# Kernel optimization log

Hardware: AMD Instinct MI355X
Metric: run time of the kernel (lower is better)

Reference implementation:

```python
import jax, jax.numpy as jnp
import numpy as np

D_LOGIC = 256
D_MEMORY = 256
NHEAD = 4
B, S = 2, 4096


def setup_inputs() -> dict:
    key = jax.random.key(0)
    ks = jax.random.split(key, 12)
    scale = 0.02
    x_logic = jax.random.normal(ks[0], (B, S, D_LOGIC), dtype=jnp.float32)
    x_memory = jax.random.normal(ks[1], (B, S, D_MEMORY), dtype=jnp.float32)
    mask = jax.random.randint(ks[2], (1, 1, S, S), 0, 2, dtype=jnp.int32)
    # torch nn.Linear weights are [out_features, in_features]
    Wq = jax.random.normal(ks[3], (D_LOGIC, D_LOGIC), dtype=jnp.float32) * scale
    bq = jnp.zeros((D_LOGIC,), dtype=jnp.float32)
    Wk = jax.random.normal(ks[4], (D_LOGIC, D_LOGIC), dtype=jnp.float32) * scale
    bk = jnp.zeros((D_LOGIC,), dtype=jnp.float32)
    Wv = jax.random.normal(ks[5], (D_MEMORY, D_MEMORY), dtype=jnp.float32) * scale
    bv = jnp.zeros((D_MEMORY,), dtype=jnp.float32)
    Wo = jax.random.normal(ks[6], (D_MEMORY, D_MEMORY), dtype=jnp.float32) * scale
    bo = jnp.zeros((D_MEMORY,), dtype=jnp.float32)
    return {"x_logic": x_logic, "x_memory": x_memory, "mask": mask,
            "Wq": Wq, "bq": bq, "Wk": Wk, "bk": bk,
            "Wv": Wv, "bv": bv, "Wo": Wo, "bo": bo}


def reference(x_logic, x_memory, mask, Wq, bq, Wk, bk, Wv, bv, Wo, bo):
    batch, seq, _ = x_logic.shape
    hd_l = D_LOGIC // NHEAD   # head_dim_logic
    hd_m = D_MEMORY // NHEAD  # head_dim_memory
    # Q, K from logic stream
    Q = (x_logic @ Wq.T + bq).reshape(batch, seq, NHEAD, hd_l)
    K = (x_logic @ Wk.T + bk).reshape(batch, seq, NHEAD, hd_l)
    # scores: [B, H, S, S]
    scores = jnp.einsum('bqhd,bkhd->bhqk', Q, K) / jnp.sqrt(jnp.float32(hd_l))
    scores = jnp.where(mask == 0, jnp.float32(-1e9), scores)
    attn = jax.nn.softmax(scores, axis=-1)
    # V from memory stream
    V = (x_memory @ Wv.T + bv).reshape(batch, seq, NHEAD, hd_m)
    out = jnp.einsum('bhqk,bkhd->bqhd', attn, V).reshape(batch, seq, D_MEMORY)
    return out @ Wo.T + bo
```

## Files before the change

kernel.cpp:

```cpp
#include <hip/hip_runtime.h>

#define S_  4096
#define HD_ 64
#define H_  4
#define B_  2
#define DM  256
#define NS  4
#define KSPAN (S_ / NS)
#define NITER (KSPAN / 64)

typedef __bf16 bf16x8 __attribute__((ext_vector_type(8)));
typedef __bf16 bf16x4 __attribute__((ext_vector_type(4)));
typedef float  f32x4  __attribute__((ext_vector_type(4)));
typedef unsigned long long u64;

__device__ __forceinline__ bf16x8 cvt8(const float* p) {
    float4 u0 = *reinterpret_cast<const float4*>(p);
    float4 u1 = *reinterpret_cast<const float4*>(p + 4);
    bf16x8 r = { (__bf16)u0.x, (__bf16)u0.y, (__bf16)u0.z, (__bf16)u0.w,
                 (__bf16)u1.x, (__bf16)u1.y, (__bf16)u1.z, (__bf16)u1.w };
    return r;
}

__global__ __launch_bounds__(256) void pack_kernel(const int* __restrict__ mask,
                                                   u64* __restrict__ packed,
                                                   const float* __restrict__ Wq,
                                                   const float* __restrict__ Wk,
                                                   const float* __restrict__ Wv,
                                                   const float* __restrict__ Wo,
                                                   __bf16* __restrict__ wqb,
                                                   __bf16* __restrict__ wkb,
                                                   __bf16* __restrict__ wvb,
                                                   __bf16* __restrict__ wob) {
    const int bid = blockIdx.x;
    if (bid < 1024) {
        const int gw   = bid * 4 + (threadIdx.x >> 6);
        const int lane = threadIdx.x & 63;
        const int r  = lane >> 4;
        const int ll = lane & 15;
#pragma unroll
        for (int s = 0; s < 16; ++s) {
            const int u   = gw + s * 4096;
            const int kbb = u & 63;
            const int q0  = (u >> 6) * 4;
            const int4 v = *reinterpret_cast<const int4*>(
                mask + (size_t)(q0 + r) * S_ + kbb * 64 + ll * 4);
            const u64 b0 = __ballot(v.x != 0);
            const u64 b1 = __ballot(v.y != 0);
            const u64 b2 = __ballot(v.z != 0);
            const u64 b3 = __ballot(v.w != 0);
            if (ll == 0) {
                const u64 word = ((b0 >> (16 * r)) & 0xFFFFull)
                               | (((b1 >> (16 * r)) & 0xFFFFull) << 16)
                               | (((b2 >> (16 * r)) & 0xFFFFull) << 32)
                               | (((b3 >> (16 * r)) & 0xFFFFull) << 48);
                packed[(size_t)kbb * S_ + q0 + r] = word;
            }
        }
        return;
    }
    const int t = (bid - 1024) * 256 + threadIdx.x;
#pragma unroll
    for (int j = 0; j < 4; ++j) {
        const int idx = t + j * 16384;
        const int arr = idx >> 14, k = idx & 16383;
        const float* src = arr == 0 ? Wq : arr == 1 ? Wk : arr == 2 ? Wv : Wo;
        __bf16* dst      = arr == 0 ? wqb : arr == 1 ? wkb : arr == 2 ? wvb : wob;
        float4 v = reinterpret_cast<const float4*>(src)[k];
        bf16x4 o = { (__bf16)v.x, (__bf16)v.y, (__bf16)v.z, (__bf16)v.w };
        reinterpret_cast<bf16x4*>(dst)[k] = o;
    }
}

__global__ __launch_bounds__(256) void proj_qkv_kernel(const float* __restrict__ xl,
                                                       const float* __restrict__ xm,
                                                       const __bf16* __restrict__ wqb,
                                                       const __bf16* __restrict__ wkb,
                                                       const __bf16* __restrict__ wvb,
                                                       const float* __restrict__ bq,
                                                       const float* __restrict__ bk,
                                                       const float* __restrict__ bv,
                                                       __bf16* __restrict__ Qb,
                                                       __bf16* __restrict__ Kb,
                                                       __bf16* __restrict__ Vtb) {
    const int mode = blockIdx.z;
    const int ny   = blockIdx.y;
    const float*  X    = (mode == 2) ? xm : xl;
    const __bf16* W    = (mode == 0) ? wqb : (mode == 1) ? wkb : wvb;
    const float*  bias = (mode == 0) ? bq : (mode == 1) ? bk : bv;
    const float scale  = (mode == 0) ? 0.18033688011112042f : 1.0f;

    const int wid  = threadIdx.x >> 6;
    const int lane = threadIdx.x & 63;
    const int g = lane >> 4, c = lane & 15;
    const int m0 = blockIdx.x * 64 + wid * 16;
    const float* Xp = X + (size_t)m0 * DM;

    f32x4 acc[8];
#pragma unroll
    for (int i = 0; i < 8; ++i) acc[i] = (f32x4){0.f, 0.f, 0.f, 0.f};

#pragma unroll
    for (int kf = 0; kf < 8; ++kf) {
        bf16x8 a = cvt8(Xp + c * DM + kf * 32 + g * 8);
#pragma unroll
        for (int nt = 0; nt < 8; ++nt) {
            bf16x8 b = *reinterpret_cast<const bf16x8*>(
                W + (size_t)(ny * 128 + nt * 16 + c) * DM + kf * 32 + g * 8);
            acc[nt] = __builtin_amdgcn_mfma_f32_16x16x32_bf16(a, b, acc[nt], 0, 0, 0);
        }
    }

#pragma unroll
    for (int nt = 0; nt < 8; ++nt) {
        const int n = ny * 128 + nt * 16 + c;
        const float bs = bias[n];
        const int h = n >> 6, d = n & 63;
#pragma unroll
        for (int r = 0; r < 4; ++r) {
            const int m = m0 + g * 4 + r;
            const float v = (acc[nt][r] + bs) * scale;
            const int b_ = m >> 12, s = m & (S_ - 1);
            if (mode == 0)
                Qb[((size_t)(b_ * H_ + h) * S_ + s) * HD_ + d] = (__bf16)v;
            else if (mode == 1)
                Kb[((size_t)(b_ * H_ + h) * S_ + s) * HD_ + d] = (__bf16)v;
            else
                Vtb[((size_t)(b_ * H_ + h) * HD_ + d) * S_ + s] = (__bf16)v;
        }
    }
}

__global__ __launch_bounds__(256, 4) void attn_kernel(const __bf16* __restrict__ Q,
                                                      const __bf16* __restrict__ K,
                                                      const __bf16* __restrict__ Vt,
                                                      const u64* __restrict__ packed,
                                                      __bf16* __restrict__ Opart,
                                                      float* __restrict__ Lpart) {
    __shared__ __bf16 Kt[64][72];
    __shared__ __bf16 Vl[64][72];
    __shared__ __bf16 Pl[4][16][72];

    const int bh = blockIdx.x;
    const int sp = blockIdx.y;
    const int qt = blockIdx.z;
    const int tid  = threadIdx.x;
    const int wid  = tid >> 6;
    const int lane = tid & 63;
    const int g = lane >> 4, c = lane & 15;
    const int q0w = qt * 64 + wid * 16;

    const __bf16* Qp = Q + ((size_t)bh * S_ + q0w) * HD_;
    bf16x8 qb0 = *reinterpret_cast<const bf16x8*>(Qp + c * HD_ + g * 8);
    bf16x8 qb1 = *reinterpret_cast<const bf16x8*>(Qp + c * HD_ + 32 + g * 8);

    const __bf16* Kp = K  + (size_t)bh * S_ * HD_;
    const __bf16* Vp = Vt + (size_t)bh * HD_ * S_;

    const int srow = tid >> 2;
    const int sseg = (tid & 3) * 16;

    f32x4 o[4];
#pragma unroll
    for (int i = 0; i < 4; ++i) o[i] = (f32x4){0.f, 0.f, 0.f, 0.f};
    float rs = 0.f;

    const int k0 = sp * KSPAN;

    bf16x8 kr0, kr1, vr0, vr1;
    {
        const __bf16* krow = Kp + (size_t)(k0 + srow) * HD_ + sseg;
        const __bf16* vrow = Vp + (size_t)srow * S_ + k0 + sseg;
        kr0 = *reinterpret_cast<const bf16x8*>(krow);
        kr1 = *reinterpret_cast<const bf16x8*>(krow + 8);
        vr0 = *reinterpret_cast<const bf16x8*>(vrow);
        vr1 = *reinterpret_cast<const bf16x8*>(vrow + 8);
        *reinterpret_cast<bf16x8*>(&Kt[srow][sseg])     = kr0;
        *reinterpret_cast<bf16x8*>(&Kt[srow][sseg + 8]) = kr1;
        *reinterpret_cast<bf16x8*>(&Vl[srow][sseg])     = vr0;
        *reinterpret_cast<bf16x8*>(&Vl[srow][sseg + 8]) = vr1;
    }
    __syncthreads();

    for (int it = 0; it < NITER; ++it) {
        const int kb = k0 + it * 64;
        const bool more = (it + 1 < NITER);
        if (more) {
            const __bf16* krow = Kp + (size_t)(kb + 64 + srow) * HD_ + sseg;
            const __bf16* vrow = Vp + (size_t)srow * S_ + kb + 64 + sseg;
            kr0 = *reinterpret_cast<const bf16x8*>(krow);
            kr1 = *reinterpret_cast<const bf16x8*>(krow + 8);
            vr0 = *reinterpret_cast<const bf16x8*>(vrow);
            vr1 = *reinterpret_cast<const bf16x8*>(vrow + 8);
        }

        const u64 mw = packed[(size_t)(kb >> 6) * S_ + q0w + c];
        const unsigned wlo = (unsigned)mw, whi = (unsigned)(mw >> 32);

        f32x4 st[4];
#pragma unroll
        for (int nt = 0; nt < 4; ++nt) {
            bf16x8 ka0 = *reinterpret_cast<const bf16x8*>(&Kt[nt * 16 + c][g * 8]);
            bf16x8 ka1 = *reinterpret_cast<const bf16x8*>(&Kt[nt * 16 + c][32 + g * 8]);
            f32x4 z = (f32x4){0.f, 0.f, 0.f, 0.f};
            st[nt] = __builtin_amdgcn_mfma_f32_16x16x32_bf16(ka0, qb0, z, 0, 0, 0);
            st[nt] = __builtin_amdgcn_mfma_f32_16x16x32_bf16(ka1, qb1, st[nt], 0, 0, 0);
        }

#pragma unroll
        for (int nt = 0; nt < 4; ++nt) {
            const unsigned sh = nt * 4 + g;
            float p0 = ((wlo >> sh) & 1u)        ? exp2f(st[nt][0]) : 0.f;
            float p1 = ((wlo >> (sh + 16)) & 1u) ? exp2f(st[nt][1]) : 0.f;
            float p2 = ((whi >> sh) & 1u)        ? exp2f(st[nt][2]) : 0.f;
            float p3 = ((whi >> (sh + 16)) & 1u) ? exp2f(st[nt][3]) : 0.f;
            rs += (p0 + p1) + (p2 + p3);
            bf16x4 pw = { (__bf16)p0, (__bf16)p1, (__bf16)p2, (__bf16)p3 };
            *reinterpret_cast<bf16x4*>(&Pl[wid][c][nt * 16 + g * 4]) = pw;
        }

        bf16x8 pa0 = *reinterpret_cast<const bf16x8*>(&Pl[wid][c][g * 8]);
        bf16x8 pa1 = *reinterpret_cast<const bf16x8*>(&Pl[wid][c][32 + g * 8]);

#pragma unroll
        for (int nt = 0; nt < 4; ++nt) {
            bf16x8 vb0 = *reinterpret_cast<const bf16x8*>(&Vl[nt * 16 + c][g * 8]);
            bf16x8 vb1 = *reinterpret_cast<const bf16x8*>(&Vl[nt * 16 + c][32 + g * 8]);
            o[nt] = __builtin_amdgcn_mfma_f32_16x16x32_bf16(pa0, vb0, o[nt], 0, 0, 0);
            o[nt] = __builtin_amdgcn_mfma_f32_16x16x32_bf16(pa1, vb1, o[nt], 0, 0, 0);
        }

        __syncthreads();
        if (more) {
            *reinterpret_cast<bf16x8*>(&Kt[srow][sseg])     = kr0;
            *reinterpret_cast<bf16x8*>(&Kt[srow][sseg + 8]) = kr1;
            *reinterpret_cast<bf16x8*>(&Vl[srow][sseg])     = vr0;
            *reinterpret_cast<bf16x8*>(&Vl[srow][sseg + 8]) = vr1;
            __syncthreads();
        }
    }

    rs += __shfl_xor(rs, 16);
    rs += __shfl_xor(rs, 32);
    if (lane < 16)
        Lpart[(size_t)(bh * NS + sp) * S_ + q0w + c] = rs;

    const size_t obase = ((size_t)(bh * NS + sp) * S_ + q0w) * 64;
#pragma unroll
    for (int nt = 0; nt < 4; ++nt) {
#pragma unroll
        for (int r = 0; r < 4; ++r)
            Opart[obase + (size_t)(g * 4 + r) * 64 + nt * 16 + c] = (__bf16)o[nt][r];
    }
}

__global__ __launch_bounds__(256) void proj_o_kernel(const __bf16* __restrict__ Opart,
                                                     const float* __restrict__ Lpart,
                                                     const __bf16* __restrict__ wob,
                                                     const float* __restrict__ bo,
                                                     float* __restrict__ out) {
    const int ny   = blockIdx.y;
    const int wid  = threadIdx.x >> 6;
    const int lane = threadIdx.x & 63;
    const int g = lane >> 4, c = lane & 15;
    const int m0 = blockIdx.x * 64 + wid * 16;

    const int row = m0 + c;
    const int b_ = row >> 12, s = row & (S_ - 1);

    f32x4 acc[8];
#pragma unroll
    for (int i = 0; i < 8; ++i) acc[i] = (f32x4){0.f, 0.f, 0.f, 0.f};

#pragma unroll
    for (int kf = 0; kf < 8; ++kf) {
        const int dcol = kf * 32 + g * 8;
        const int h = dcol >> 6, dm = dcol & 63;
        const int bh = b_ * H_ + h;
        float l = 0.f;
        float sum[8] = {0.f, 0.f, 0.f, 0.f, 0.f, 0.f, 0.f, 0.f};
#pragma unroll
        for (int sp = 0; sp < NS; ++sp) {
            l += Lpart[(size_t)(bh * NS + sp) * S_ + s];
            const size_t base = ((size_t)(bh * NS + sp) * S_ + s) * 64 + dm;
            bf16x8 p = *reinterpret_cast<const bf16x8*>(Opart + base);
#pragma unroll
            for (int j = 0; j < 8; ++j) sum[j] += (float)p[j];
        }
        const float invl = 1.0f / l;
        bf16x8 a = { (__bf16)(sum[0] * invl), (__bf16)(sum[1] * invl),
                     (__bf16)(sum[2] * invl), (__bf16)(sum[3] * invl),
                     (__bf16)(sum[4] * invl), (__bf16)(sum[5] * invl),
                     (__bf16)(sum[6] * invl), (__bf16)(sum[7] * invl) };
#pragma unroll
        for (int nt = 0; nt < 8; ++nt) {
            bf16x8 b = *reinterpret_cast<const bf16x8*>(
                wob + (size_t)(ny * 128 + nt * 16 + c) * DM + kf * 32 + g * 8);
            acc[nt] = __builtin_amdgcn_mfma_f32_16x16x32_bf16(a, b, acc[nt], 0, 0, 0);
        }
    }

#pragma unroll
    for (int nt = 0; nt < 8; ++nt) {
        const int n = ny * 128 + nt * 16 + c;
        const float bs = bo[n];
#pragma unroll
        for (int r = 0; r < 4; ++r) {
            const int m = m0 + g * 4 + r;
            out[(size_t)m * DM + n] = acc[nt][r] + bs;
        }
    }
}

extern "C" void kernel_launch(void* const* d_in, const int* in_sizes, int n_in,
                              void* d_out, int out_size, void* d_ws, size_t ws_size,
                              hipStream_t stream) {
    const float* x_logic  = (const float*)d_in[0];
    const float* x_memory = (const float*)d_in[1];
    const int*   mask     = (const int*)d_in[2];
    const float* Wq = (const float*)d_in[3];
    const float* bq = (const float*)d_in[4];
    const float* Wk = (const float*)d_in[5];
    const float* bk = (const float*)d_in[6];
    const float* Wv = (const float*)d_in[7];
    const float* bv = (const float*)d_in[8];
    const float* Wo = (const float*)d_in[9];
    const float* bo = (const float*)d_in[10];
    float* out = (float*)d_out;

    char* ws = (char*)d_ws;
    size_t off = 0;
    auto alloc = [&](size_t bytes) { char* p = ws + off; off += (bytes + 255) & ~255ull; return p; };

    const size_t NX = (size_t)B_ * S_ * DM;
    u64*    packed = (u64*)alloc((size_t)S_ * (S_ / 64) * 8);
    __bf16* wqb = (__bf16*)alloc((size_t)DM * DM * 2);
    __bf16* wkb = (__bf16*)alloc((size_t)DM * DM * 2);
    __bf16* wvb = (__bf16*)alloc((size_t)DM * DM * 2);
    __bf16* wob = (__bf16*)alloc((size_t)DM * DM * 2);
    __bf16* Qb  = (__bf16*)alloc(NX * 2);
    __bf16* Kb  = (__bf16*)alloc(NX * 2);
    __bf16* Vtb = (__bf16*)alloc(NX * 2);
    __bf16* Opart = (__bf16*)alloc((size_t)B_ * H_ * NS * S_ * HD_ * 2);
    float*  Lpart = (float*)alloc((size_t)B_ * H_ * NS * S_ * 4);

    pack_kernel<<<1088, 256, 0, stream>>>(mask, packed, Wq, Wk, Wv, Wo, wqb, wkb, wvb, wob);
    proj_qkv_kernel<<<dim3(128, 2, 3), 256, 0, stream>>>(x_logic, x_memory, wqb, wkb, wvb,
                                                         bq, bk, bv, Qb, Kb, Vtb);
    attn_kernel<<<dim3(8, NS, 64), 256, 0, stream>>>(Qb, Kb, Vtb, packed, Opart, Lpart);
    proj_o_kernel<<<dim3(128, 2), 256, 0, stream>>>(Opart, Lpart, wob, bo, out);
}
```

Measured before the change: 138.7 us.

## Double-buffer K/V tiles in LDS with one barrier per iteration

The attention kernel now keeps two LDS buffers for the K and V tiles. While the current tile is being computed, the next tile's registers are stored into the other buffer and the tile after that is prefetched from global memory. This cuts the barriers per iteration from two to one and gives global loads a longer lead time. It also adds s_setprio around the MFMA sections, and the mask pack kernel now batches four loads before doing the ballots. In exchange, LDS use doubles, which may reduce occupancy, and register pressure goes up.

```diff
diff --git a/kernel.cpp b/kernel.cpp
--- a/kernel.cpp
+++ b/kernel.cpp
@@ -39,22 +39,32 @@
         const int r  = lane >> 4;
         const int ll = lane & 15;
 #pragma unroll
-        for (int s = 0; s < 16; ++s) {
-            const int u   = gw + s * 4096;
-            const int kbb = u & 63;
-            const int q0  = (u >> 6) * 4;
-            const int4 v = *reinterpret_cast<const int4*>(
-                mask + (size_t)(q0 + r) * S_ + kbb * 64 + ll * 4);
-            const u64 b0 = __ballot(v.x != 0);
-            const u64 b1 = __ballot(v.y != 0);
-            const u64 b2 = __ballot(v.z != 0);
-            const u64 b3 = __ballot(v.w != 0);
-            if (ll == 0) {
-                const u64 word = ((b0 >> (16 * r)) & 0xFFFFull)
-                               | (((b1 >> (16 * r)) & 0xFFFFull) << 16)
-                               | (((b2 >> (16 * r)) & 0xFFFFull) << 32)
-                               | (((b3 >> (16 * r)) & 0xFFFFull) << 48);
-                packed[(size_t)kbb * S_ + q0 + r] = word;
+        for (int sb = 0; sb < 4; ++sb) {
+            int4 v[4];
+#pragma unroll
+            for (int j = 0; j < 4; ++j) {
+                const int u   = gw + (sb * 4 + j) * 4096;
+                const int kbb = u & 63;
+                const int q0  = (u >> 6) * 4;
+                v[j] = *reinterpret_cast<const int4*>(
+                    mask + (size_t)(q0 + r) * S_ + kbb * 64 + ll * 4);
+            }
+#pragma unroll
+            for (int j = 0; j < 4; ++j) {
+                const int u   = gw + (sb * 4 + j) * 4096;
+                const int kbb = u & 63;
+                const int q0  = (u >> 6) * 4;
+                const u64 b0 = __ballot(v[j].x != 0);
+                const u64 b1 = __ballot(v[j].y != 0);
+                const u64 b2 = __ballot(v[j].z != 0);
+                const u64 b3 = __ballot(v[j].w != 0);
+                if (ll == 0) {
+                    const u64 word = ((b0 >> (16 * r)) & 0xFFFFull)
+                                   | (((b1 >> (16 * r)) & 0xFFFFull) << 16)
+                                   | (((b2 >> (16 * r)) & 0xFFFFull) << 32)
+                                   | (((b3 >> (16 * r)) & 0xFFFFull) << 48);
+                    packed[(size_t)kbb * S_ + q0 + r] = word;
+                }
             }
         }
         return;
@@ -137,8 +147,8 @@
                                                       const u64* __restrict__ packed,
                                                       __bf16* __restrict__ Opart,
                                                       float* __restrict__ Lpart) {
-    __shared__ __bf16 Kt[64][72];
-    __shared__ __bf16 Vl[64][72];
+    __shared__ __bf16 Kt[2][64][72];
+    __shared__ __bf16 Vl[2][64][72];
     __shared__ __bf16 Pl[4][16][72];
 
     const int bh = blockIdx.x;
@@ -166,46 +176,60 @@
     float rs = 0.f;
 
     const int k0 = sp * KSPAN;
-
-    bf16x8 kr0, kr1, vr0, vr1;
+    const __bf16* kptr = Kp + (size_t)(k0 + srow) * HD_ + sseg;
+    const __bf16* vptr = Vp + (size_t)srow * S_ + k0 + sseg;
+
     {
-        const __bf16* krow = Kp + (size_t)(k0 + srow) * HD_ + sseg;
-        const __bf16* vrow = Vp + (size_t)srow * S_ + k0 + sseg;
-        kr0 = *reinterpret_cast<const bf16x8*>(krow);
-        kr1 = *reinterpret_cast<const bf16x8*>(krow + 8);
-        vr0 = *reinterpret_cast<const bf16x8*>(vrow);
-        vr1 = *reinterpret_cast<const bf16x8*>(vrow + 8);
-        *reinterpret_cast<bf16x8*>(&Kt[srow][sseg])     = kr0;
-        *reinterpret_cast<bf16x8*>(&Kt[srow][sseg + 8]) = kr1;
-        *reinterpret_cast<bf16x8*>(&Vl[srow][sseg])     = vr0;
-        *reinterpret_cast<bf16x8*>(&Vl[srow][sseg + 8]) = vr1;
-    }
+        bf16x8 a0 = *reinterpret_cast<const bf16x8*>(kptr);
+        bf16x8 a1 = *reinterpret_cast<const bf16x8*>(kptr + 8);
+        bf16x8 b0 = *reinterpret_cast<const bf16x8*>(vptr);
+        bf16x8 b1 = *reinterpret_cast<const bf16x8*>(vptr + 8);
+        *reinterpret_cast<bf16x8*>(&Kt[0][srow][sseg])     = a0;
+        *reinterpret_cast<bf16x8*>(&Kt[0][srow][sseg + 8]) = a1;
+        *reinterpret_cast<bf16x8*>(&Vl[0][srow][sseg])     = b0;
+        *reinterpret_cast<bf16x8*>(&Vl[0][srow][sseg + 8]) = b1;
+    }
+    kptr += (size_t)64 * HD_;
+    vptr += 64;
+    bf16x8 kr0 = *reinterpret_cast<const bf16x8*>(kptr);
+    bf16x8 kr1 = *reinterpret_cast<const bf16x8*>(kptr + 8);
+    bf16x8 vr0 = *reinterpret_cast<const bf16x8*>(vptr);
+    bf16x8 vr1 = *reinterpret_cast<const bf16x8*>(vptr + 8);
     __syncthreads();
 
     for (int it = 0; it < NITER; ++it) {
+        const int cur = it & 1;
         const int kb = k0 + it * 64;
-        const bool more = (it + 1 < NITER);
-        if (more) {
-            const __bf16* krow = Kp + (size_t)(kb + 64 + srow) * HD_ + sseg;
-            const __bf16* vrow = Vp + (size_t)srow * S_ + kb + 64 + sseg;
-            kr0 = *reinterpret_cast<const bf16x8*>(krow);
-            kr1 = *reinterpret_cast<const bf16x8*>(krow + 8);
-            vr0 = *reinterpret_cast<const bf16x8*>(vrow);
-            vr1 = *reinterpret_cast<const bf16x8*>(vrow + 8);
+
+        if (it + 1 < NITER) {
+            *reinterpret_cast<bf16x8*>(&Kt[cur ^ 1][srow][sseg])     = kr0;
+            *reinterpret_cast<bf16x8*>(&Kt[cur ^ 1][srow][sseg + 8]) = kr1;
+            *reinterpret_cast<bf16x8*>(&Vl[cur ^ 1][srow][sseg])     = vr0;
+            *reinterpret_cast<bf16x8*>(&Vl[cur ^ 1][srow][sseg + 8]) = vr1;
+        }
+        if (it + 2 < NITER) {
+            kptr += (size_t)64 * HD_;
+            vptr += 64;
+            kr0 = *reinterpret_cast<const bf16x8*>(kptr);
+            kr1 = *reinterpret_cast<const bf16x8*>(kptr + 8);
+            vr0 = *reinterpret_cast<const bf16x8*>(vptr);
+            vr1 = *reinterpret_cast<const bf16x8*>(vptr + 8);
         }
 
         const u64 mw = packed[(size_t)(kb >> 6) * S_ + q0w + c];
         const unsigned wlo = (unsigned)mw, whi = (unsigned)(mw >> 32);
 
         f32x4 st[4];
+        __builtin_amdgcn_s_setprio(1);
 #pragma unroll
         for (int nt = 0; nt < 4; ++nt) {
-            bf16x8 ka0 = *reinterpret_cast<const bf16x8*>(&Kt[nt * 16 + c][g * 8]);
-            bf16x8 ka1 = *reinterpret_cast<const bf16x8*>(&Kt[nt * 16 + c][32 + g * 8]);
+            bf16x8 ka0 = *reinterpret_cast<const bf16x8*>(&Kt[cur][nt * 16 + c][g * 8]);
+            bf16x8 ka1 = *reinterpret_cast<const bf16x8*>(&Kt[cur][nt * 16 + c][32 + g * 8]);
             f32x4 z = (f32x4){0.f, 0.f, 0.f, 0.f};
             st[nt] = __builtin_amdgcn_mfma_f32_16x16x32_bf16(ka0, qb0, z, 0, 0, 0);
             st[nt] = __builtin_amdgcn_mfma_f32_16x16x32_bf16(ka1, qb1, st[nt], 0, 0, 0);
         }
+        __builtin_amdgcn_s_setprio(0);
 
 #pragma unroll
         for (int nt = 0; nt < 4; ++nt) {
@@ -222,22 +246,17 @@
         bf16x8 pa0 = *reinterpret_cast<const bf16x8*>(&Pl[wid][c][g * 8]);
         bf16x8 pa1 = *reinterpret_cast<const bf16x8*>(&Pl[wid][c][32 + g * 8]);
 
+        __builtin_amdgcn_s_setprio(1);
 #pragma unroll
         for (int nt = 0; nt < 4; ++nt) {
-            bf16x8 vb0 = *reinterpret_cast<const bf16x8*>(&Vl[nt * 16 + c][g * 8]);
-            bf16x8 vb1 = *reinterpret_cast<const bf16x8*>(&Vl[nt * 16 + c][32 + g * 8]);
+            bf16x8 vb0 = *reinterpret_cast<const bf16x8*>(&Vl[cur][nt * 16 + c][g * 8]);
+            bf16x8 vb1 = *reinterpret_cast<const bf16x8*>(&Vl[cur][nt * 16 + c][32 + g * 8]);
             o[nt] = __builtin_amdgcn_mfma_f32_16x16x32_bf16(pa0, vb0, o[nt], 0, 0, 0);
             o[nt] = __builtin_amdgcn_mfma_f32_16x16x32_bf16(pa1, vb1, o[nt], 0, 0, 0);
         }
-
-        __syncthreads();
-        if (more) {
-            *reinterpret_cast<bf16x8*>(&Kt[srow][sseg])     = kr0;
-            *reinterpret_cast<bf16x8*>(&Kt[srow][sseg + 8]) = kr1;
-            *reinterpret_cast<bf16x8*>(&Vl[srow][sseg])     = vr0;
-            *reinterpret_cast<bf16x8*>(&Vl[srow][sseg + 8]) = vr1;
-            __syncthreads();
-        }
+        __builtin_amdgcn_s_setprio(0);
+
+        if (it + 1 < NITER) __syncthreads();
     }
 
     rs += __shfl_xor(rs, 16);
```

Result: slower. 144.8 us (+4.3%).

## Process two query sub-tiles per wave in attention and batch mask loads

Applied to the files above, without the earlier changes.

Each attention wave now handles 32 query rows instead of 16, so every K/V tile staged in shared memory feeds twice as many MFMAs. The grid's query dimension is halved to match. This cuts global-to-LDS traffic and sync overhead per unit of work, at the cost of more registers per wave and fewer blocks to spread across CUs. Separately, the mask-packing loop now issues four int4 loads before doing the ballots, giving more memory-level parallelism.

```diff
diff --git a/kernel.cpp b/kernel.cpp
--- a/kernel.cpp
+++ b/kernel.cpp
@@ -39,22 +39,32 @@
         const int r  = lane >> 4;
         const int ll = lane & 15;
 #pragma unroll
-        for (int s = 0; s < 16; ++s) {
-            const int u   = gw + s * 4096;
-            const int kbb = u & 63;
-            const int q0  = (u >> 6) * 4;
-            const int4 v = *reinterpret_cast<const int4*>(
-                mask + (size_t)(q0 + r) * S_ + kbb * 64 + ll * 4);
-            const u64 b0 = __ballot(v.x != 0);
-            const u64 b1 = __ballot(v.y != 0);
-            const u64 b2 = __ballot(v.z != 0);
-            const u64 b3 = __ballot(v.w != 0);
-            if (ll == 0) {
-                const u64 word = ((b0 >> (16 * r)) & 0xFFFFull)
-                               | (((b1 >> (16 * r)) & 0xFFFFull) << 16)
-                               | (((b2 >> (16 * r)) & 0xFFFFull) << 32)
-                               | (((b3 >> (16 * r)) & 0xFFFFull) << 48);
-                packed[(size_t)kbb * S_ + q0 + r] = word;
+        for (int sb = 0; sb < 4; ++sb) {
+            int4 v[4];
+#pragma unroll
+            for (int j = 0; j < 4; ++j) {
+                const int u   = gw + (sb * 4 + j) * 4096;
+                const int kbb = u & 63;
+                const int q0  = (u >> 6) * 4;
+                v[j] = *reinterpret_cast<const int4*>(
+                    mask + (size_t)(q0 + r) * S_ + kbb * 64 + ll * 4);
+            }
+#pragma unroll
+            for (int j = 0; j < 4; ++j) {
+                const int u   = gw + (sb * 4 + j) * 4096;
+                const int kbb = u & 63;
+                const int q0  = (u >> 6) * 4;
+                const u64 b0 = __ballot(v[j].x != 0);
+                const u64 b1 = __ballot(v[j].y != 0);
+                const u64 b2 = __ballot(v[j].z != 0);
+                const u64 b3 = __ballot(v[j].w != 0);
+                if (ll == 0) {
+                    const u64 word = ((b0 >> (16 * r)) & 0xFFFFull)
+                                   | (((b1 >> (16 * r)) & 0xFFFFull) << 16)
+                                   | (((b2 >> (16 * r)) & 0xFFFFull) << 32)
+                                   | (((b3 >> (16 * r)) & 0xFFFFull) << 48);
+                    packed[(size_t)kbb * S_ + q0 + r] = word;
+                }
             }
         }
         return;
@@ -139,7 +149,7 @@
                                                       float* __restrict__ Lpart) {
     __shared__ __bf16 Kt[64][72];
     __shared__ __bf16 Vl[64][72];
-    __shared__ __bf16 Pl[4][16][72];
+    __shared__ __bf16 Pl[4][32][72];
 
     const int bh = blockIdx.x;
     const int sp = blockIdx.y;
@@ -148,11 +158,15 @@
     const int wid  = tid >> 6;
     const int lane = tid & 63;
     const int g = lane >> 4, c = lane & 15;
-    const int q0w = qt * 64 + wid * 16;
+    const int q0w = qt * 128 + wid * 32;
 
     const __bf16* Qp = Q + ((size_t)bh * S_ + q0w) * HD_;
-    bf16x8 qb0 = *reinterpret_cast<const bf16x8*>(Qp + c * HD_ + g * 8);
-    bf16x8 qb1 = *reinterpret_cast<const bf16x8*>(Qp + c * HD_ + 32 + g * 8);
+    bf16x8 qb[2][2];
+#pragma unroll
+    for (int qh = 0; qh < 2; ++qh) {
+        qb[qh][0] = *reinterpret_cast<const bf16x8*>(Qp + (qh * 16 + c) * HD_ + g * 8);
+        qb[qh][1] = *reinterpret_cast<const bf16x8*>(Qp + (qh * 16 + c) * HD_ + 32 + g * 8);
+    }
 
     const __bf16* Kp = K  + (size_t)bh * S_ * HD_;
     const __bf16* Vp = Vt + (size_t)bh * HD_ * S_;
@@ -160,10 +174,12 @@
     const int srow = tid >> 2;
     const int sseg = (tid & 3) * 16;
 
-    f32x4 o[4];
-#pragma unroll
-    for (int i = 0; i < 4; ++i) o[i] = (f32x4){0.f, 0.f, 0.f, 0.f};
-    float rs = 0.f;
+    f32x4 o[2][4];
+#pragma unroll
+    for (int qh = 0; qh < 2; ++qh)
+#pragma unroll
+        for (int i = 0; i < 4; ++i) o[qh][i] = (f32x4){0.f, 0.f, 0.f, 0.f};
+    float rs[2] = {0.f, 0.f};
 
     const int k0 = sp * KSPAN;
 
@@ -194,40 +210,55 @@
             vr1 = *reinterpret_cast<const bf16x8*>(vrow + 8);
         }
 
-        const u64 mw = packed[(size_t)(kb >> 6) * S_ + q0w + c];
-        const unsigned wlo = (unsigned)mw, whi = (unsigned)(mw >> 32);
-
-        f32x4 st[4];
+        const u64 mwA = packed[(size_t)(kb >> 6) * S_ + q0w + c];
+        const u64 mwB = packed[(size_t)(kb >> 6) * S_ + q0w + 16 + c];
+
+        f32x4 st[4][2];
 #pragma unroll
         for (int nt = 0; nt < 4; ++nt) {
             bf16x8 ka0 = *reinterpret_cast<const bf16x8*>(&Kt[nt * 16 + c][g * 8]);
             bf16x8 ka1 = *reinterpret_cast<const bf16x8*>(&Kt[nt * 16 + c][32 + g * 8]);
-            f32x4 z = (f32x4){0.f, 0.f, 0.f, 0.f};
-            st[nt] = __builtin_amdgcn_mfma_f32_16x16x32_bf16(ka0, qb0, z, 0, 0, 0);
-            st[nt] = __builtin_amdgcn_mfma_f32_16x16x32_bf16(ka1, qb1, st[nt], 0, 0, 0);
-        }
-
-#pragma unroll
-        for (int nt = 0; nt < 4; ++nt) {
-            const unsigned sh = nt * 4 + g;
-            float p0 = ((wlo >> sh) & 1u)        ? exp2f(st[nt][0]) : 0.f;
-            float p1 = ((wlo >> (sh + 16)) & 1u) ? exp2f(st[nt][1]) : 0.f;
-            float p2 = ((whi >> sh) & 1u)        ? exp2f(st[nt][2]) : 0.f;
-            float p3 = ((whi >> (sh + 16)) & 1u) ? exp2f(st[nt][3]) : 0.f;
-            rs += (p0 + p1) + (p2 + p3);
-            bf16x4 pw = { (__bf16)p0, (__bf16)p1, (__bf16)p2, (__bf16)p3 };
-            *reinterpret_cast<bf16x4*>(&Pl[wid][c][nt * 16 + g * 4]) = pw;
-        }
-
-        bf16x8 pa0 = *reinterpret_cast<const bf16x8*>(&Pl[wid][c][g * 8]);
-        bf16x8 pa1 = *reinterpret_cast<const bf16x8*>(&Pl[wid][c][32 + g * 8]);
+#pragma unroll
+            for (int qh = 0; qh < 2; ++qh) {
+                f32x4 z = (f32x4){0.f, 0.f, 0.f, 0.f};
+                st[nt][qh] = __builtin_amdgcn_mfma_f32_16x16x32_bf16(ka0, qb[qh][0], z, 0, 0, 0);
+                st[nt][qh] = __builtin_amdgcn_mfma_f32_16x16x32_bf16(ka1, qb[qh][1], st[nt][qh], 0, 0, 0);
+            }
+        }
+
+#pragma unroll
+        for (int qh = 0; qh < 2; ++qh) {
+            const u64 mw = qh ? mwB : mwA;
+            const unsigned wlo = (unsigned)mw, whi = (unsigned)(mw >> 32);
+#pragma unroll
+            for (int nt = 0; nt < 4; ++nt) {
+                const unsigned sh = nt * 4 + g;
+                float p0 = ((wlo >> sh) & 1u)        ? exp2f(st[nt][qh][0]) : 0.f;
+                float p1 = ((wlo >> (sh + 16)) & 1u) ? exp2f(st[nt][qh][1]) : 0.f;
+                float p2 = ((whi >> sh) & 1u)        ? exp2f(st[nt][qh][2]) : 0.f;
+                float p3 = ((whi >> (sh + 16)) & 1u) ? exp2f(st[nt][qh][3]) : 0.f;
+                rs[qh] += (p0 + p1) + (p2 + p3);
+                bf16x4 pw = { (__bf16)p0, (__bf16)p1, (__bf16)p2, (__bf16)p3 };
+                *reinterpret_cast<bf16x4*>(&Pl[wid][qh * 16 + c][nt * 16 + g * 4]) = pw;
+            }
+        }
+
+        bf16x8 pa[2][2];
+#pragma unroll
+        for (int qh = 0; qh < 2; ++qh) {
+            pa[qh][0] = *reinterpret_cast<const bf16x8*>(&Pl[wid][qh * 16 + c][g * 8]);
+            pa[qh][1] = *reinterpret_cast<const bf16x8*>(&Pl[wid][qh * 16 + c][32 + g * 8]);
+        }
 
 #pragma unroll
         for (int nt = 0; nt < 4; ++nt) {
             bf16x8 vb0 = *reinterpret_cast<const bf16x8*>(&Vl[nt * 16 + c][g * 8]);
             bf16x8 vb1 = *reinterpret_cast<const bf16x8*>(&Vl[nt * 16 + c][32 + g * 8]);
-            o[nt] = __builtin_amdgcn_mfma_f32_16x16x32_bf16(pa0, vb0, o[nt], 0, 0, 0);
-            o[nt] = __builtin_amdgcn_mfma_f32_16x16x32_bf16(pa1, vb1, o[nt], 0, 0, 0);
+#pragma unroll
+            for (int qh = 0; qh < 2; ++qh) {
+                o[qh][nt] = __builtin_amdgcn_mfma_f32_16x16x32_bf16(pa[qh][0], vb0, o[qh][nt], 0, 0, 0);
+                o[qh][nt] = __builtin_amdgcn_mfma_f32_16x16x32_bf16(pa[qh][1], vb1, o[qh][nt], 0, 0, 0);
+            }
         }
 
         __syncthreads();
@@ -240,17 +271,25 @@
         }
     }
 
-    rs += __shfl_xor(rs, 16);
-    rs += __shfl_xor(rs, 32);
-    if (lane < 16)
-        Lpart[(size_t)(bh * NS + sp) * S_ + q0w + c] = rs;
-
-    const size_t obase = ((size_t)(bh * NS + sp) * S_ + q0w) * 64;
-#pragma unroll
-    for (int nt = 0; nt < 4; ++nt) {
-#pragma unroll
-        for (int r = 0; r < 4; ++r)
-            Opart[obase + (size_t)(g * 4 + r) * 64 + nt * 16 + c] = (__bf16)o[nt][r];
+#pragma unroll
+    for (int qh = 0; qh < 2; ++qh) {
+        rs[qh] += __shfl_xor(rs[qh], 16);
+        rs[qh] += __shfl_xor(rs[qh], 32);
+    }
+    if (lane < 16) {
+        Lpart[(size_t)(bh * NS + sp) * S_ + q0w + c]      = rs[0];
+        Lpart[(size_t)(bh * NS + sp) * S_ + q0w + 16 + c] = rs[1];
+    }
+
+#pragma unroll
+    for (int qh = 0; qh < 2; ++qh) {
+        const size_t obase = ((size_t)(bh * NS + sp) * S_ + q0w + qh * 16) * 64;
+#pragma unroll
+        for (int nt = 0; nt < 4; ++nt) {
+#pragma unroll
+            for (int r = 0; r < 4; ++r)
+                Opart[obase + (size_t)(g * 4 + r) * 64 + nt * 16 + c] = (__bf16)o[qh][nt][r];
+        }
     }
 }
 
@@ -347,6 +386,6 @@
     pack_kernel<<<1088, 256, 0, stream>>>(mask, packed, Wq, Wk, Wv, Wo, wqb, wkb, wvb, wob);
     proj_qkv_kernel<<<dim3(128, 2, 3), 256, 0, stream>>>(x_logic, x_memory, wqb, wkb, wvb,
                                                          bq, bk, bv, Qb, Kb, Vtb);
-    attn_kernel<<<dim3(8, NS, 64), 256, 0, stream>>>(Qb, Kb, Vtb, packed, Opart, Lpart);
+    attn_kernel<<<dim3(8, NS, 32), 256, 0, stream>>>(Qb, Kb, Vtb, packed, Opart, Lpart);
     proj_o_kernel<<<dim3(128, 2), 256, 0, stream>>>(Opart, Lpart, wob, bo, out);
 }
```

Result: faster. 135.0 us (-2.7%).
